# Performance work log

Hardware: AMD Instinct MI355X
Metric: run time of the kernel (lower is better)

The kernel has to match this reference:

```python
import jax, jax.numpy as jnp
import numpy as np

N = 200000   # 10000 graphs x 20 nodes, stacked
E = 3200000  # avg degree 16
F_IN = 4
H = 32
BN_EPS = 1e-5


def setup_inputs() -> dict:
    key = jax.random.key(0)
    ks = jax.random.split(key, 16)
    s = 0.1
    return {
        "x": jax.random.normal(ks[0], (N, F_IN), jnp.float32),
        "edge_index": jax.random.randint(ks[1], (2, E), 0, N, jnp.int64),
        "edge_weight": jax.random.uniform(ks[2], (E,), jnp.float32),
        "gcn1_w": jax.random.normal(ks[3], (F_IN, H), jnp.float32) * s,
        "gcn1_b": jnp.zeros((H,), jnp.float32),
        "gcn2_w": jax.random.normal(ks[4], (H, H), jnp.float32) * s,
        "gcn2_b": jnp.zeros((H,), jnp.float32),
        "bn1_gamma": jnp.ones((H,), jnp.float32),
        "bn1_beta": jnp.zeros((H,), jnp.float32),
        "bn1_mean": jnp.zeros((H,), jnp.float32),
        "bn1_var": jnp.ones((H,), jnp.float32),
        "bn2_gamma": jnp.ones((H,), jnp.float32),
        "bn2_beta": jnp.zeros((H,), jnp.float32),
        "bn2_mean": jnp.zeros((H,), jnp.float32),
        "bn2_var": jnp.ones((H,), jnp.float32),
        "lstm1_wih": jax.random.normal(ks[5], (4 * H, 2 * H), jnp.float32) * s,
        "lstm1_whh": jax.random.normal(ks[6], (4 * H, H), jnp.float32) * s,
        "lstm1_bih": jax.random.normal(ks[7], (4 * H,), jnp.float32) * s,
        "lstm1_bhh": jax.random.normal(ks[8], (4 * H,), jnp.float32) * s,
        "lstm2_wih": jax.random.normal(ks[9], (4 * H, H), jnp.float32) * s,
        "lstm2_whh": jax.random.normal(ks[10], (4 * H, H), jnp.float32) * s,
        "lstm2_bih": jax.random.normal(ks[11], (4 * H,), jnp.float32) * s,
        "lstm2_bhh": jax.random.normal(ks[12], (4 * H,), jnp.float32) * s,
        "lin_w": jax.random.normal(ks[13], (1, 2 * H + F_IN), jnp.float32) * s,
        "lin_b": jnp.zeros((1,), jnp.float32),
    }


def _gcn_conv(x, src, dst, ew, W, b, n):
    # GCNConv: x @ W, add self-loops (weight 1), symmetric normalization, scatter-add at dst.
    xw = x @ W
    loop = jnp.arange(n)
    s = jnp.concatenate([src, loop])
    d = jnp.concatenate([dst, loop])
    w = jnp.concatenate([ew, jnp.ones((n,), ew.dtype)])
    deg = jax.ops.segment_sum(w, d, num_segments=n)
    dinv = jnp.where(deg > 0, jax.lax.rsqrt(deg), 0.0)
    norm = dinv[s] * w * dinv[d]  # [E+N]
    out = jax.ops.segment_sum(norm[:, None] * xw[s], d, num_segments=n)
    return out + b


def _bn_eval(x, gamma, beta, mean, var):
    return (x - mean) * jax.lax.rsqrt(var + BN_EPS) * gamma + beta


def _lstm_step(x, wih, bih, bhh):
    # single timestep, zero initial (h, c): recurrent W_hh term vanishes.
    gates = x @ wih.T + bih + bhh
    i, f, g, o = jnp.split(gates, 4, axis=1)  # torch gate order i,f,g,o
    c = jax.nn.sigmoid(i) * jnp.tanh(g)
    return jax.nn.sigmoid(o) * jnp.tanh(c)


def reference(x, edge_index, edge_weight, gcn1_w, gcn1_b, gcn2_w, gcn2_b,
              bn1_gamma, bn1_beta, bn1_mean, bn1_var,
              bn2_gamma, bn2_beta, bn2_mean, bn2_var,
              lstm1_wih, lstm1_whh, lstm1_bih, lstm1_bhh,
              lstm2_wih, lstm2_whh, lstm2_bih, lstm2_bhh,
              lin_w, lin_b):
    n = x.shape[0]
    src, dst = edge_index[0], edge_index[1]
    # MPNNLSTM (window=1, eval mode: dropout=identity, BN uses running stats)
    h1 = _bn_eval(jax.nn.relu(_gcn_conv(x, src, dst, edge_weight, gcn1_w, gcn1_b, n)),
                  bn1_gamma, bn1_beta, bn1_mean, bn1_var)
    h2 = _bn_eval(jax.nn.relu(_gcn_conv(h1, src, dst, edge_weight, gcn2_w, gcn2_b, n)),
                  bn2_gamma, bn2_beta, bn2_mean, bn2_var)
    skip = jnp.concatenate([h1, h2], axis=1)  # [N, 2H]
    H1 = _lstm_step(skip, lstm1_wih, lstm1_bih, lstm1_bhh)  # [N, H]
    H2 = _lstm_step(H1, lstm2_wih, lstm2_bih, lstm2_bhh)    # [N, H]
    h = jnp.concatenate([H1, H2, x], axis=1)  # [N, 2H + F_IN]
    # RecurrentGCN head: relu + linear -> [N, 1]
    return jax.nn.relu(h) @ lin_w.T + lin_b
```

## Files before the change

kernel.cpp:

```cpp
#include <hip/hip_runtime.h>
#include <hip/hip_fp16.h>
#include <math.h>

#define BN_EPS 1e-5f
#define HF 32
#define BS 256
#define KEDGE 4096
#define MAXNB 800
#define WQ14 16383.0f
#define WQ22 4194303.0f

typedef _Float16 half8 __attribute__((ext_vector_type(8)));
typedef float f32x4 __attribute__((ext_vector_type(4)));
typedef float f32x2 __attribute__((ext_vector_type(2)));

__device__ __forceinline__ float fsig(float x) {
    return __builtin_amdgcn_rcpf(1.0f + __expf(-x));
}
__device__ __forceinline__ float ftanh(float x) {
    return 1.0f - 2.0f * __builtin_amdgcn_rcpf(1.0f + __expf(2.0f * x));
}


__device__ __forceinline__ float e4m3_to_f32_sw(unsigned v) {
    unsigned s = v & 0x80u, E = (v >> 3) & 0xFu, m = v & 7u;
    float r = E ? ldexpf((float)(8 + m), (int)E - 10) : ldexpf((float)m, -9);
    return s ? -r : r;
}

__device__ __forceinline__ unsigned f32_to_e4m3_sw(float x) {
    float ax = fabsf(x);
    unsigned s = x < 0.0f ? 0x80u : 0u;
    if (!(ax > 0.0f)) return s;
    if (ax >= 448.0f) return s | 0x7Eu;
    int e;
    float m = frexpf(ax, &e);
    int E = e - 1 + 7;
    if (E >= 1) {
        int q = (int)(m * 16.0f + 0.5f);
        if (q == 16) { q = 8; E += 1; if (E > 15) return s | 0x7Eu; }
        return s | (unsigned)(E << 3) | (unsigned)(q - 8);
    }
    int q = (int)(ax * 512.0f + 0.5f);
    if (q > 7) return s | 0x08u;
    return s | (unsigned)q;
}

__device__ __forceinline__ void dec8(uint2 r, float* f) {
#if __has_builtin(__builtin_amdgcn_cvt_pk_f32_fp8)
    f32x2 p0 = __builtin_amdgcn_cvt_pk_f32_fp8((int)r.x, false);
    f32x2 p1 = __builtin_amdgcn_cvt_pk_f32_fp8((int)r.x, true);
    f32x2 p2 = __builtin_amdgcn_cvt_pk_f32_fp8((int)r.y, false);
    f32x2 p3 = __builtin_amdgcn_cvt_pk_f32_fp8((int)r.y, true);
    f[0] = p0[0]; f[1] = p0[1]; f[2] = p1[0]; f[3] = p1[1];
    f[4] = p2[0]; f[5] = p2[1]; f[6] = p3[0]; f[7] = p3[1];
#else
#pragma unroll
    for (int k = 0; k < 4; ++k) f[k] = e4m3_to_f32_sw((r.x >> (8 * k)) & 0xFFu);
#pragma unroll
    for (int k = 0; k < 4; ++k) f[4 + k] = e4m3_to_f32_sw((r.y >> (8 * k)) & 0xFFu);
#endif
}

__device__ __forceinline__ uint2 enc8(const float* o) {
#if __has_builtin(__builtin_amdgcn_cvt_pk_fp8_f32)
    int w0 = 0, w1 = 0;
    w0 = __builtin_amdgcn_cvt_pk_fp8_f32(o[0], o[1], w0, false);
    w0 = __builtin_amdgcn_cvt_pk_fp8_f32(o[2], o[3], w0, true);
    w1 = __builtin_amdgcn_cvt_pk_fp8_f32(o[4], o[5], w1, false);
    w1 = __builtin_amdgcn_cvt_pk_fp8_f32(o[6], o[7], w1, true);
    return make_uint2((unsigned)w0, (unsigned)w1);
#else
    unsigned a = 0, b = 0;
#pragma unroll
    for (int k = 0; k < 4; ++k) a |= f32_to_e4m3_sw(o[k]) << (8 * k);
#pragma unroll
    for (int k = 0; k < 4; ++k) b |= f32_to_e4m3_sw(o[4 + k]) << (8 * k);
    return make_uint2(a, b);
#endif
}


__global__ __launch_bounds__(512) void k_binsort(
        const int* __restrict__ src, const int* __restrict__ dst,
        const float* __restrict__ ew, int E, int NB, int bcap,
        int* __restrict__ gcur, uint2* __restrict__ recs) {
    __shared__ uint2 srec[KEDGE];
    __shared__ int hist[MAXNB], excl[MAXNB], curs[MAXNB], sbase[MAXNB];

    int tid = threadIdx.x;
    int base = blockIdx.x * KEDGE;
    int cnt = min(KEDGE, E - base);

    for (int i = tid; i < NB; i += 512) hist[i] = 0;
    __syncthreads();

    for (int i = tid; i < cnt; i += 512)
        atomicAdd(&hist[dst[base + i] >> 8], 1);
    __syncthreads();

    if (tid < 64) {
        int run = 0;
        for (int c = 0; c < NB; c += 64) {
            int idx = c + tid;
            int v = (idx < NB) ? hist[idx] : 0;
            int incl = v;
#pragma unroll
            for (int o = 1; o < 64; o <<= 1) {
                int up = __shfl_up(incl, o, 64);
                if (tid >= o) incl += up;
            }
            if (idx < NB) { int e = run + incl - v; excl[idx] = e; curs[idx] = e; }
            run += __shfl(incl, 63, 64);
        }
    }
    __syncthreads();

    for (int i = tid; i < cnt; i += 512) {
        int s = src[base + i];
        int d = dst[base + i];
        float w = ew[base + i];
        unsigned q = (unsigned)(w * WQ22 + 0.5f);
        if (q > 4194303u) q = 4194303u;
        int b = d >> 8;
        int pos = atomicAdd(&curs[b], 1);
        srec[pos] = make_uint2(((unsigned)s << 8) | (unsigned)(d & 255),
                               ((unsigned)b << 22) | q);
    }
    __syncthreads();

    for (int b = tid; b < NB; b += 512) {
        int len = hist[b];
        sbase[b] = len ? atomicAdd(&gcur[b], len) : 0;
    }
    __syncthreads();

    for (int i = tid; i < cnt; i += 512) {
        uint2 u = srec[i];
        int b = u.y >> 22;
        int off = sbase[b] + (i - excl[b]);
        if (off < bcap) recs[(size_t)b * bcap + off] = u;
    }
}


__global__ __launch_bounds__(512) void k_sortb(
        const uint2* __restrict__ recs, const int* __restrict__ gcur,
        int bcap, int bcap4,
        const float* __restrict__ x, const float* __restrict__ W1,
        unsigned* __restrict__ recs4, int* __restrict__ pstart,
        int* __restrict__ pcnt, float* __restrict__ dinv,
        unsigned char* __restrict__ y18, int n) {
    __shared__ int hist[BS], excl4[BS], curs[BS], wsm[BS];
    __shared__ float sdv[BS];
    __shared__ float sW1[128];

    int b = blockIdx.x, tid = threadIdx.x;
    int cnt = min(gcur[b], bcap);
    const uint2* r = recs + (size_t)b * bcap;
    const float dq = 1.0f / WQ22;

    if (tid < BS) { hist[tid] = 0; wsm[tid] = 0; }
    if (tid >= 256 && tid < 384) sW1[tid - 256] = W1[tid - 256];
    __syncthreads();

    for (int i = tid; i < cnt; i += 512) {
        uint2 u = r[i];
        int dl = u.x & 255;
        atomicAdd(&hist[dl], 1);
        atomicAdd(&wsm[dl], (int)(u.y & 4194303u));
    }
    __syncthreads();

    if (tid < BS) {
        int g = b * BS + tid;
        sdv[tid] = (g < n) ? rsqrtf(1.0f + (float)wsm[tid] * dq) : 0.0f;
    }
    if (tid < 64) {
        int run = 0;
        for (int c = 0; c < BS; c += 64) {
            int idx = c + tid;
            int v = (hist[idx] + 3) & ~3;
            int incl = v;
#pragma unroll
            for (int o = 1; o < 64; o <<= 1) {
                int up = __shfl_up(incl, o, 64);
                if (tid >= o) incl += up;
            }
            int e = run + incl - v;
            excl4[idx] = e; curs[idx] = e;
            run += __shfl(incl, 63, 64);
        }
    }
    __syncthreads();

    unsigned* out4 = recs4 + (size_t)b * bcap4;
    for (int i = tid; i < cnt; i += 512) {
        uint2 u = r[i];
        int dl = u.x & 255;
        int pos = atomicAdd(&curs[dl], 1);
        float qn = (float)(u.y & 4194303u) * dq * sdv[dl];
        unsigned q = (unsigned)(qn * WQ14 + 0.5f);
        if (q > 16383u) q = 16383u;
        out4[pos] = ((u.x >> 8) << 14) | q;
    }

    {
        int node = tid >> 1, half = tid & 1;
        int g = b * BS + node;
        if (g < n) {
            float4 xv = *(const float4*)(x + (size_t)g * 4);
            float sc = sdv[node];
            int f0 = half * 16;
            float o[16];
#pragma unroll
            for (int k = 0; k < 16; ++k)
                o[k] = sc * (xv.x * sW1[f0 + k] + xv.y * sW1[32 + f0 + k] +
                             xv.z * sW1[64 + f0 + k] + xv.w * sW1[96 + f0 + k]);
            uint2 lo = enc8(o), hi = enc8(o + 8);
            *(uint4*)(y18 + ((size_t)g << 5) + half * 16) = make_uint4(lo.x, lo.y, hi.x, hi.y);
        }
    }

    if (tid < BS) {
        int g = b * BS + tid;
        if (g < n) {
            pstart[g] = b * bcap4 + excl4[tid];
            pcnt[g] = hist[tid];
            dinv[g] = sdv[tid];
        }
    }
}


__global__ __launch_bounds__(256) void k_prep(
        const float* __restrict__ wih1, const float* __restrict__ bih1,
        const float* __restrict__ bhh1, const float* __restrict__ wih2,
        const float* __restrict__ bih2, const float* __restrict__ bhh2,
        __half* __restrict__ wp1, __half* __restrict__ wp2,
        float* __restrict__ bsum1, float* __restrict__ bsum2,
        int* __restrict__ gcur, int NB) {
    const int tg[6] = {0, 16, 64, 80, 96, 112};
    int idx = blockIdx.x * 256 + threadIdx.x;
    if (idx < 6144) {
        int t = idx >> 10, rem = idx & 1023;
        int kc = rem >> 9, rem2 = rem & 511;
        int lane = rem2 >> 3, j = rem2 & 7;
        int g = tg[t] + (lane & 15);
        int k = kc * 32 + (lane >> 4) * 8 + j;
        wp1[idx] = __float2half(wih1[g * 64 + k]);
    } else if (idx < 9216) {
        int i2 = idx - 6144;
        int t = i2 >> 9, rem2 = i2 & 511;
        int lane = rem2 >> 3, j = rem2 & 7;
        int g = tg[t] + (lane & 15);
        int k = (lane >> 4) * 8 + j;
        wp2[i2] = __float2half(wih2[g * 32 + k]);
    } else if (idx < 9344) {
        int i = idx - 9216;
        bsum1[i] = bih1[i] + bhh1[i];
    } else if (idx < 9472) {
        int i = idx - 9344;
        bsum2[i] = bih2[i] + bhh2[i];
    } else if (idx < 9472 + NB) {
        gcur[idx - 9472] = 0;
    }
}


__global__ __launch_bounds__(256) void k_g1w2(
        const unsigned* __restrict__ recs4, const int* __restrict__ pstart,
        const int* __restrict__ pcnt, const float* __restrict__ dinv,
        const unsigned char* __restrict__ y18, const float* __restrict__ W2,
        const float* __restrict__ bias, const float* __restrict__ gamma,
        const float* __restrict__ beta, const float* __restrict__ mean,
        const float* __restrict__ var,
        __half* __restrict__ skiph, unsigned char* __restrict__ A8, int n) {
    __shared__ float sW2[1024];
    __shared__ float sh1[64][33];
    int tid = threadIdx.x;
    for (int i = tid; i < 1024; i += 256) sW2[i] = W2[i];
    __syncthreads();

    int nl = tid >> 2;
    int g = blockIdx.x * 64 + nl;
    int lane = tid & 3;
    int fq = lane * 8;
    bool act = g < n;

    float acc[8];
#pragma unroll
    for (int k = 0; k < 8; ++k) acc[k] = 0.0f;

    float dig = 0.0f;
    if (act) {
        dig = dinv[g];
        {
            uint2 sr = ((const uint2*)(y18 + ((size_t)g << 5)))[lane];
            float f[8];
            dec8(sr, f);
#pragma unroll
            for (int k = 0; k < 8; ++k) acc[k] = dig * f[k];
        }

        const float qs = 1.0f / WQ14;
        int cn = pcnt[g];
        const unsigned* r = recs4 + pstart[g];
        int e = 0;
        for (; e + 8 <= cn; e += 8) {
            uint4 ua = *(const uint4*)(r + e);
            uint4 ub = *(const uint4*)(r + e + 4);
            unsigned u[8] = {ua.x, ua.y, ua.z, ua.w, ub.x, ub.y, ub.z, ub.w};
            uint2 rw[8];
#pragma unroll
            for (int q = 0; q < 8; ++q)
                rw[q] = ((const uint2*)(y18 + ((size_t)(u[q] >> 14) << 5)))[lane];
            float nm[8];
#pragma unroll
            for (int q = 0; q < 8; ++q)
                nm[q] = (float)(u[q] & 16383u) * qs;
#pragma unroll
            for (int q = 0; q < 8; ++q) {
                float f[8];
                dec8(rw[q], f);
#pragma unroll
                for (int k = 0; k < 8; ++k) acc[k] += nm[q] * f[k];
            }
        }
        for (; e < cn; ++e) {
            unsigned u0 = r[e];
            uint2 r0 = ((const uint2*)(y18 + ((size_t)(u0 >> 14) << 5)))[lane];
            float n0 = (float)(u0 & 16383u) * qs;
            float f[8];
            dec8(r0, f);
#pragma unroll
            for (int k = 0; k < 8; ++k) acc[k] += n0 * f[k];
        }
    }

    float o[8];
#pragma unroll
    for (int k = 0; k < 8; ++k) {
        float v = fmaxf(acc[k] + bias[fq + k], 0.0f);
        o[k] = (v - mean[fq + k]) * gamma[fq + k] * rsqrtf(var[fq + k] + BN_EPS) + beta[fq + k];
        sh1[nl][fq + k] = o[k];
    }
    if (act) {
        union { __half h[8]; uint4 q; } hv;
#pragma unroll
        for (int k = 0; k < 8; ++k) hv.h[k] = __float2half(o[k]);
        *(uint4*)(skiph + (size_t)g * 64 + fq) = hv.q;
    }
    __syncthreads();

    if (act) {
        float a2[8];
#pragma unroll
        for (int j = 0; j < 8; ++j) a2[j] = 0.0f;
#pragma unroll 4
        for (int k = 0; k < 32; ++k) {
            float h = sh1[nl][k];
            const float* wr = sW2 + k * 32 + fq;
#pragma unroll
            for (int j = 0; j < 8; ++j) a2[j] += h * wr[j];
        }
#pragma unroll
        for (int j = 0; j < 8; ++j) a2[j] *= dig;
        ((uint2*)(A8 + ((size_t)g << 5)))[lane] = enc8(a2);
    }
}


__global__ __launch_bounds__(256) void k_gather8(
        const unsigned* __restrict__ recs4, const int* __restrict__ pstart,
        const int* __restrict__ pcnt, const float* __restrict__ dinv,
        const unsigned char* __restrict__ A8,
        const float* __restrict__ bias, const float* __restrict__ gamma,
        const float* __restrict__ beta, const float* __restrict__ mean,
        const float* __restrict__ var,
        __half* __restrict__ skiph, int uoff, int n) {
    int g = blockIdx.x * 64 + (threadIdx.x >> 2);
    int lane = threadIdx.x & 3;
    if (g >= n) return;

    float dig = dinv[g];
    float acc[8];
    {
        uint2 sr = ((const uint2*)(A8 + ((size_t)g << 5)))[lane];
        float f[8];
        dec8(sr, f);
#pragma unroll
        for (int k = 0; k < 8; ++k) acc[k] = dig * f[k];
    }

    const float qs = 1.0f / WQ14;
    int cn = pcnt[g];
    const unsigned* r = recs4 + pstart[g];
    int e = 0;
    for (; e + 8 <= cn; e += 8) {
        uint4 ua = *(const uint4*)(r + e);
        uint4 ub = *(const uint4*)(r + e + 4);
        unsigned u[8] = {ua.x, ua.y, ua.z, ua.w, ub.x, ub.y, ub.z, ub.w};
        uint2 rw[8];
#pragma unroll
        for (int q = 0; q < 8; ++q)
            rw[q] = ((const uint2*)(A8 + ((size_t)(u[q] >> 14) << 5)))[lane];
        float nm[8];
#pragma unroll
        for (int q = 0; q < 8; ++q)
            nm[q] = (float)(u[q] & 16383u) * qs;
#pragma unroll
        for (int q = 0; q < 8; ++q) {
            float f[8];
            dec8(rw[q], f);
#pragma unroll
            for (int k = 0; k < 8; ++k) acc[k] += nm[q] * f[k];
        }
    }
    for (; e < cn; ++e) {
        unsigned u0 = r[e];
        uint2 r0 = ((const uint2*)(A8 + ((size_t)(u0 >> 14) << 5)))[lane];
        float n0 = (float)(u0 & 16383u) * qs;
        float f0[8];
        dec8(r0, f0);
#pragma unroll
        for (int k = 0; k < 8; ++k) acc[k] += n0 * f0[k];
    }

    int fq = lane * 8;
    union { __half h[8]; uint4 q; } hv;
#pragma unroll
    for (int k = 0; k < 8; ++k) {
        float v = fmaxf(acc[k] + bias[fq + k], 0.0f);
        hv.h[k] = __float2half((v - mean[fq + k]) * gamma[fq + k] * rsqrtf(var[fq + k] + BN_EPS) + beta[fq + k]);
    }
    *(uint4*)(skiph + (size_t)g * 64 + uoff + fq) = hv.q;
}


__global__ __launch_bounds__(256) void k_headm(
        const __half* __restrict__ skiph, const float* __restrict__ x,
        const __half* __restrict__ wp1, const __half* __restrict__ wp2,
        const float* __restrict__ bsum1, const float* __restrict__ bsum2,
        const float* __restrict__ lw, const float* __restrict__ lb,
        float* __restrict__ out, int n) {
    __shared__ __align__(16) __half H1lds[4 * 16 * 40];
    int tid = threadIdx.x;
    int w = tid >> 6, l = tid & 63;
    int quad = l >> 4, c = l & 15;
    int node_base = blockIdx.x * 64 + w * 16;

    int arow = node_base + c; if (arow > n - 1) arow = n - 1;
    const half8* ap = (const half8*)(skiph + (size_t)arow * 64);
    half8 a0 = ap[quad];
    half8 a1 = ap[4 + quad];

    const half8* b1 = (const half8*)wp1;
    f32x4 d[6];
#pragma unroll
    for (int t = 0; t < 6; ++t) {
        f32x4 acc = {0.0f, 0.0f, 0.0f, 0.0f};
        acc = __builtin_amdgcn_mfma_f32_16x16x32_f16(a0, b1[(t * 2 + 0) * 64 + l], acc, 0, 0, 0);
        acc = __builtin_amdgcn_mfma_f32_16x16x32_f16(a1, b1[(t * 2 + 1) * 64 + l], acc, 0, 0, 0);
        d[t] = acc;
    }

    float bi0 = bsum1[c],      bi1 = bsum1[16 + c];
    float bg0 = bsum1[64 + c], bg1 = bsum1[80 + c];
    float bo0 = bsum1[96 + c], bo1 = bsum1[112 + c];
    float lwc0 = lw[c], lwc1 = lw[c + 16];

    float pa[4];
#pragma unroll
    for (int r = 0; r < 4; ++r) {
        float cc0 = fsig(d[0][r] + bi0) * ftanh(d[2][r] + bg0);
        float h0 = fsig(d[4][r] + bo0) * ftanh(cc0);
        float cc1 = fsig(d[1][r] + bi1) * ftanh(d[3][r] + bg1);
        float h1 = fsig(d[5][r] + bo1) * ftanh(cc1);
        pa[r] = fmaxf(h0, 0.0f) * lwc0 + fmaxf(h1, 0.0f) * lwc1;
        __half* hp = H1lds + (w * 16 + quad * 4 + r) * 40;
        hp[c] = __float2half(h0);
        hp[c + 16] = __float2half(h1);
    }
    __syncthreads();

    half8 a2 = *(const half8*)(H1lds + (w * 16 + c) * 40 + quad * 8);

    const half8* b2 = (const half8*)wp2;
    f32x4 e[6];
#pragma unroll
    for (int t = 0; t < 6; ++t) {
        f32x4 acc = {0.0f, 0.0f, 0.0f, 0.0f};
        e[t] = __builtin_amdgcn_mfma_f32_16x16x32_f16(a2, b2[t * 64 + l], acc, 0, 0, 0);
    }

    float ci0 = bsum2[c],      ci1 = bsum2[16 + c];
    float cg0 = bsum2[64 + c], cg1 = bsum2[80 + c];
    float co0 = bsum2[96 + c], co1 = bsum2[112 + c];
    float lw2c0 = lw[32 + c], lw2c1 = lw[48 + c];
#pragma unroll
    for (int r = 0; r < 4; ++r) {
        float cc0 = fsig(e[0][r] + ci0) * ftanh(e[2][r] + cg0);
        float h0 = fsig(e[4][r] + co0) * ftanh(cc0);
        float cc1 = fsig(e[1][r] + ci1) * ftanh(e[3][r] + cg1);
        float h1 = fsig(e[5][r] + co1) * ftanh(cc1);
        pa[r] += fmaxf(h0, 0.0f) * lw2c0 + fmaxf(h1, 0.0f) * lw2c1;
    }

#pragma unroll
    for (int m = 1; m < 16; m <<= 1) {
#pragma unroll
        for (int r = 0; r < 4; ++r) pa[r] += __shfl_xor(pa[r], m, 64);
    }

    if (c < 4) {
        int node = node_base + quad * 4 + c;
        if (node < n) {
            const float4 xv = *(const float4*)(x + (size_t)node * 4);
            out[node] = pa[c] + lb[0]
                + fmaxf(xv.x, 0.0f) * lw[64] + fmaxf(xv.y, 0.0f) * lw[65]
                + fmaxf(xv.z, 0.0f) * lw[66] + fmaxf(xv.w, 0.0f) * lw[67];
        }
    }
}


__global__ void k_initdeg(float* __restrict__ deg, int n) {
    int i = blockIdx.x * blockDim.x + threadIdx.x;
    if (i < n) deg[i] = 1.0f;
}

__global__ void k_deg_only(const int* __restrict__ dst, const float* __restrict__ ew,
                           float* __restrict__ deg, int E) {
    int e = blockIdx.x * blockDim.x + threadIdx.x;
    if (e < E) atomicAdd(&deg[dst[e]], ew[e]);
}

__global__ void k_dinv_f(float* __restrict__ deg, int n) {
    int i = blockIdx.x * blockDim.x + threadIdx.x;
    if (i < n) {
        float d = deg[i];
        deg[i] = d > 0.0f ? rsqrtf(d) : 0.0f;
    }
}

__global__ void k_xw1_f(const float* __restrict__ x, const float* __restrict__ W,
                        float* __restrict__ out, int n) {
    int idx = blockIdx.x * blockDim.x + threadIdx.x;
    if (idx >= n * HF) return;
    int nn = idx >> 5, f = idx & 31;
    const float4 xr = *(const float4*)(x + (size_t)nn * 4);
    out[idx] = xr.x * W[f] + xr.y * W[32 + f] + xr.z * W[64 + f] + xr.w * W[96 + f];
}

__global__ void k_xw2_f(const float* __restrict__ Hin, const float* __restrict__ W,
                        float* __restrict__ out, int n) {
    __shared__ float sW[32 * 32];
    __shared__ float sH[8][32];
    int tid = threadIdx.x;
    for (int i = tid; i < 1024; i += 256) sW[i] = W[i];
    int r = tid >> 5, f = tid & 31;
    int nn = blockIdx.x * 8 + r;
    if (nn < n) sH[r][f] = Hin[(size_t)nn * HF + f];
    __syncthreads();
    if (nn >= n) return;
    float acc = 0.0f;
#pragma unroll
    for (int k = 0; k < 32; ++k) acc += sH[r][k] * sW[k * 32 + f];
    out[(size_t)nn * HF + f] = acc;
}

__global__ void k_selfloop(const float* __restrict__ A, const float* __restrict__ dinv,
                           float* __restrict__ B, int n) {
    int idx = blockIdx.x * blockDim.x + threadIdx.x;
    if (idx >= n * HF) return;
    int nn = idx >> 5;
    float di = dinv[nn];
    B[idx] = di * di * A[idx];
}

__global__ void k_scatter(const int* __restrict__ src, const int* __restrict__ dst,
                          const float* __restrict__ ew, const float* __restrict__ dinv,
                          const float* __restrict__ A, float* __restrict__ B, int total) {
    int idx = blockIdx.x * blockDim.x + threadIdx.x;
    if (idx >= total) return;
    int e = idx >> 5, f = idx & 31;
    int s = src[e], d = dst[e];
    float norm = dinv[s] * ew[e] * dinv[d];
    atomicAdd(&B[d * HF + f], norm * A[s * HF + f]);
}

__global__ void k_post(const float* __restrict__ B, const float* __restrict__ bias,
                       const float* __restrict__ gamma, const float* __restrict__ beta,
                       const float* __restrict__ mean, const float* __restrict__ var,
                       float* __restrict__ Hout, int n) {
    int idx = blockIdx.x * blockDim.x + threadIdx.x;
    if (idx >= n * HF) return;
    int f = idx & 31;
    float v = fmaxf(B[idx] + bias[f], 0.0f);
    float sc = gamma[f] * rsqrtf(var[f] + BN_EPS);
    Hout[idx] = (v - mean[f]) * sc + beta[f];
}

__global__ __launch_bounds__(256) void k_head(
        const float* __restrict__ h1, const float* __restrict__ h2,
        const float* __restrict__ x,
        const float* __restrict__ wih1, const float* __restrict__ bih1, const float* __restrict__ bhh1,
        const float* __restrict__ wih2, const float* __restrict__ bih2, const float* __restrict__ bhh2,
        const float* __restrict__ lw, const float* __restrict__ lb,
        float* __restrict__ out, int n) {
    __shared__ float sH1[32 * 256];
    int tid = threadIdx.x;
    int nn = blockIdx.x * 256 + tid;
    if (nn >= n) return;

    const float4* a = (const float4*)(h1 + (size_t)nn * HF);
    const float4* b = (const float4*)(h2 + (size_t)nn * HF);
    float skip[64];
#pragma unroll
    for (int q = 0; q < 8; ++q) {
        float4 v = a[q];
        skip[4 * q] = v.x; skip[4 * q + 1] = v.y; skip[4 * q + 2] = v.z; skip[4 * q + 3] = v.w;
        float4 u = b[q];
        skip[32 + 4 * q] = u.x; skip[33 + 4 * q] = u.y; skip[34 + 4 * q] = u.z; skip[35 + 4 * q] = u.w;
    }

    float oa = lb[0];
#pragma unroll 1
    for (int j = 0; j < 32; ++j) {
        const float4* wi = (const float4*)(wih1 + (size_t)j * 64);
        const float4* wg = (const float4*)(wih1 + (size_t)(64 + j) * 64);
        const float4* wo = (const float4*)(wih1 + (size_t)(96 + j) * 64);
        float gi = bih1[j] + bhh1[j];
        float gg = bih1[64 + j] + bhh1[64 + j];
        float go = bih1[96 + j] + bhh1[96 + j];
#pragma unroll
        for (int q = 0; q < 16; ++q) {
            float4 aa = wi[q], bb = wg[q], cc4 = wo[q];
            float s0 = skip[4 * q], s1 = skip[4 * q + 1], s2 = skip[4 * q + 2], s3 = skip[4 * q + 3];
            gi += aa.x * s0 + aa.y * s1 + aa.z * s2 + aa.w * s3;
            gg += bb.x * s0 + bb.y * s1 + bb.z * s2 + bb.w * s3;
            go += cc4.x * s0 + cc4.y * s1 + cc4.z * s2 + cc4.w * s3;
        }
        float cc = fsig(gi) * ftanh(gg);
        float hh = fsig(go) * ftanh(cc);
        sH1[j * 256 + tid] = hh;
        oa += fmaxf(hh, 0.0f) * lw[j];
    }

#pragma unroll 1
    for (int j = 0; j < 32; ++j) {
        const float4* wi = (const float4*)(wih2 + (size_t)j * 32);
        const float4* wg = (const float4*)(wih2 + (size_t)(64 + j) * 32);
        const float4* wo = (const float4*)(wih2 + (size_t)(96 + j) * 32);
        float gi = bih2[j] + bhh2[j];
        float gg = bih2[64 + j] + bhh2[64 + j];
        float go = bih2[96 + j] + bhh2[96 + j];
#pragma unroll
        for (int q = 0; q < 8; ++q) {
            float4 aa = wi[q], bb = wg[q], cc4 = wo[q];
            float s0 = sH1[(4 * q) * 256 + tid], s1 = sH1[(4 * q + 1) * 256 + tid];
            float s2 = sH1[(4 * q + 2) * 256 + tid], s3 = sH1[(4 * q + 3) * 256 + tid];
            gi += aa.x * s0 + aa.y * s1 + aa.z * s2 + aa.w * s3;
            gg += bb.x * s0 + bb.y * s1 + bb.z * s2 + bb.w * s3;
            go += cc4.x * s0 + cc4.y * s1 + cc4.z * s2 + cc4.w * s3;
        }
        float cc = fsig(gi) * ftanh(gg);
        float hh = fsig(go) * ftanh(cc);
        oa += fmaxf(hh, 0.0f) * lw[32 + j];
    }

    const float4 xv = *(const float4*)(x + (size_t)nn * 4);
    oa += fmaxf(xv.x, 0.0f) * lw[64] + fmaxf(xv.y, 0.0f) * lw[65] +
          fmaxf(xv.z, 0.0f) * lw[66] + fmaxf(xv.w, 0.0f) * lw[67];
    out[nn] = oa;
}


extern "C" void kernel_launch(void* const* d_in, const int* in_sizes, int n_in,
                              void* d_out, int out_size, void* d_ws, size_t ws_size,
                              hipStream_t stream) {
    const float* x   = (const float*)d_in[0];
    const int*   ei  = (const int*)d_in[1];
    const float* ew  = (const float*)d_in[2];
    const float* g1w = (const float*)d_in[3];
    const float* g1b = (const float*)d_in[4];
    const float* g2w = (const float*)d_in[5];
    const float* g2b = (const float*)d_in[6];
    const float* bn1g = (const float*)d_in[7];
    const float* bn1b = (const float*)d_in[8];
    const float* bn1m = (const float*)d_in[9];
    const float* bn1v = (const float*)d_in[10];
    const float* bn2g = (const float*)d_in[11];
    const float* bn2b = (const float*)d_in[12];
    const float* bn2m = (const float*)d_in[13];
    const float* bn2v = (const float*)d_in[14];
    const float* w1ih = (const float*)d_in[15];
    const float* b1ih = (const float*)d_in[17];
    const float* b1hh = (const float*)d_in[18];
    const float* w2ih = (const float*)d_in[19];
    const float* b2ih = (const float*)d_in[21];
    const float* b2hh = (const float*)d_in[22];
    const float* lw   = (const float*)d_in[23];
    const float* lb   = (const float*)d_in[24];
    float* out = (float*)d_out;

    const int N = in_sizes[0] / 4;
    const int E = in_sizes[2];
    const int* src = ei;
    const int* dst = ei + E;

    const int T = 256;
    const int NB = (N + BS - 1) / BS;
    long long meanb = ((long long)BS * E) / (N > 0 ? N : 1);
    int bcap = (int)(meanb + meanb / 4 + 128);
    bcap = (bcap + 3) & ~3;
    int bcap4 = bcap + 3 * BS;

    char* p = (char*)d_ws;
    auto alloc = [&](size_t bytes) { char* q = p; p += (bytes + 255) & ~(size_t)255; return q; };
    int*      gcur   = (int*)alloc(sizeof(int) * NB);
    uint2*    recs   = (uint2*)alloc(sizeof(uint2) * (size_t)NB * bcap);
    unsigned* recs4  = (unsigned*)alloc(sizeof(unsigned) * (size_t)NB * bcap4);
    float*    dinv   = (float*)alloc(sizeof(float) * N);
    int*      pstart = (int*)alloc(sizeof(int) * N);
    int*      pcnt   = (int*)alloc(sizeof(int) * N);
    unsigned char* y18 = (unsigned char*)alloc((size_t)N * HF);
    unsigned char* A8  = (unsigned char*)alloc((size_t)N * HF);
    __half*   skiph  = (__half*)alloc(sizeof(__half) * (size_t)N * 64);
    __half*   wp1    = (__half*)alloc(sizeof(__half) * 6144);
    __half*   wp2    = (__half*)alloc(sizeof(__half) * 3072);
    float*    bsum1  = (float*)alloc(sizeof(float) * 128);
    float*    bsum2  = (float*)alloc(sizeof(float) * 128);
    size_t need = (size_t)(p - (char*)d_ws);

    int bN  = (N + T - 1) / T;
    int bE  = (E + T - 1) / T;
    int bNF = (N * HF + T - 1) / T;
    int bN8 = (N + 7) / 8;
    int bG  = (N + 63) / 64;
    int bBin = (E + KEDGE - 1) / KEDGE;
    int bPrep = (9472 + NB + 255) / 256;

    if (ws_size >= need && NB <= MAXNB && N <= (1 << 18)) {
        k_prep<<<bPrep, 256, 0, stream>>>(w1ih, b1ih, b1hh, w2ih, b2ih, b2hh,
                                          wp1, wp2, bsum1, bsum2, gcur, NB);
        k_binsort<<<bBin, 512, 0, stream>>>(src, dst, ew, E, NB, bcap, gcur, recs);
        k_sortb<<<NB, 512, 0, stream>>>(recs, gcur, bcap, bcap4, x, g1w,
                                        recs4, pstart, pcnt, dinv, y18, N);

        k_g1w2<<<bG, T, 0, stream>>>(recs4, pstart, pcnt, dinv, y18, g2w,
                                     g1b, bn1g, bn1b, bn1m, bn1v, skiph, A8, N);
        k_gather8<<<bG, T, 0, stream>>>(recs4, pstart, pcnt, dinv, A8,
                                        g2b, bn2g, bn2b, bn2m, bn2v, skiph, 32, N);
        k_headm<<<bG, T, 0, stream>>>(skiph, x, wp1, wp2, bsum1, bsum2,
                                      lw, lb, out, N);
    } else {
        size_t Npad = ((size_t)N + 255) & ~(size_t)255;
        float* fdinv = (float*)d_ws;
        float* fA = fdinv + Npad;
        float* fB = fA + (size_t)N * HF;
        float* fC = fB + (size_t)N * HF;
        int bEF = (int)(((long long)E * HF + T - 1) / T);
        int bH = (N + 255) / 256;

        k_initdeg<<<bN, T, 0, stream>>>(fdinv, N);
        k_deg_only<<<bE, T, 0, stream>>>(dst, ew, fdinv, E);
        k_dinv_f<<<bN, T, 0, stream>>>(fdinv, N);

        k_xw1_f<<<bNF, T, 0, stream>>>(x, g1w, fA, N);
        k_selfloop<<<bNF, T, 0, stream>>>(fA, fdinv, fB, N);
        k_scatter<<<bEF, T, 0, stream>>>(src, dst, ew, fdinv, fA, fB, E * HF);
        k_post<<<bNF, T, 0, stream>>>(fB, g1b, bn1g, bn1b, bn1m, bn1v, fC, N);

        k_xw2_f<<<bN8, T, 0, stream>>>(fC, g2w, fA, N);
        k_selfloop<<<bNF, T, 0, stream>>>(fA, fdinv, fB, N);
        k_scatter<<<bEF, T, 0, stream>>>(src, dst, ew, fdinv, fA, fB, E * HF);
        k_post<<<bNF, T, 0, stream>>>(fB, g2b, bn2g, bn2b, bn2m, bn2v, fB, N);

        k_head<<<bH, T, 0, stream>>>(fC, fB, x, w1ih, b1ih, b1hh, w2ih, b2ih, b2hh,
                                     lw, lb, out, N);
    }
}
```

Baseline: 299.1 us.

## Bin edges via register-held records instead of LDS staging sort

The edge binning kernel now keeps each thread's 8 packed edge records in registers and reads src/dst/weight only once, building the histogram in the same pass. It drops the LDS record buffer, the wave-level prefix scan and the second global read. Scatter offsets now come from per-bin atomics on a shared cursor seeded from the global reservation. This frees about 32KB of shared memory, which should raise occupancy and cut a pass. In exchange, records within a bin are no longer grouped contiguously in shared memory, so global writes may coalesce less well and shared atomic contention rises.

```diff
diff --git a/kernel.cpp b/kernel.cpp
--- a/kernel.cpp
+++ b/kernel.cpp
@@ -85,8 +85,7 @@
         const int* __restrict__ src, const int* __restrict__ dst,
         const float* __restrict__ ew, int E, int NB, int bcap,
         int* __restrict__ gcur, uint2* __restrict__ recs) {
-    __shared__ uint2 srec[KEDGE];
-    __shared__ int hist[MAXNB], excl[MAXNB], curs[MAXNB], sbase[MAXNB];
+    __shared__ int hist[MAXNB], curs[MAXNB];
 
     int tid = threadIdx.x;
     int base = blockIdx.x * KEDGE;
@@ -95,51 +94,39 @@
     for (int i = tid; i < NB; i += 512) hist[i] = 0;
     __syncthreads();
 
-    for (int i = tid; i < cnt; i += 512)
-        atomicAdd(&hist[dst[base + i] >> 8], 1);
-    __syncthreads();
-
-    if (tid < 64) {
-        int run = 0;
-        for (int c = 0; c < NB; c += 64) {
-            int idx = c + tid;
-            int v = (idx < NB) ? hist[idx] : 0;
-            int incl = v;
-#pragma unroll
-            for (int o = 1; o < 64; o <<= 1) {
-                int up = __shfl_up(incl, o, 64);
-                if (tid >= o) incl += up;
-            }
-            if (idx < NB) { int e = run + incl - v; excl[idx] = e; curs[idx] = e; }
-            run += __shfl(incl, 63, 64);
-        }
-    }
-    __syncthreads();
-
-    for (int i = tid; i < cnt; i += 512) {
-        int s = src[base + i];
-        int d = dst[base + i];
-        float w = ew[base + i];
-        unsigned q = (unsigned)(w * WQ22 + 0.5f);
-        if (q > 4194303u) q = 4194303u;
-        int b = d >> 8;
-        int pos = atomicAdd(&curs[b], 1);
-        srec[pos] = make_uint2(((unsigned)s << 8) | (unsigned)(d & 255),
-                               ((unsigned)b << 22) | q);
+    uint2 rec[KEDGE / 512];
+#pragma unroll
+    for (int k = 0; k < KEDGE / 512; ++k) {
+        int i = tid + k * 512;
+        if (i < cnt) {
+            int s = src[base + i];
+            int d = dst[base + i];
+            float w = ew[base + i];
+            unsigned q = (unsigned)(w * WQ22 + 0.5f);
+            if (q > 4194303u) q = 4194303u;
+            int b = d >> 8;
+            rec[k] = make_uint2(((unsigned)s << 8) | (unsigned)(d & 255),
+                                ((unsigned)b << 22) | q);
+            atomicAdd(&hist[b], 1);
+        }
     }
     __syncthreads();
 
     for (int b = tid; b < NB; b += 512) {
         int len = hist[b];
-        sbase[b] = len ? atomicAdd(&gcur[b], len) : 0;
-    }
-    __syncthreads();
-
-    for (int i = tid; i < cnt; i += 512) {
-        uint2 u = srec[i];
-        int b = u.y >> 22;
-        int off = sbase[b] + (i - excl[b]);
-        if (off < bcap) recs[(size_t)b * bcap + off] = u;
+        curs[b] = len ? atomicAdd(&gcur[b], len) : 0;
+    }
+    __syncthreads();
+
+#pragma unroll
+    for (int k = 0; k < KEDGE / 512; ++k) {
+        int i = tid + k * 512;
+        if (i < cnt) {
+            uint2 u = rec[k];
+            int b = u.y >> 22;
+            int off = atomicAdd(&curs[b], 1);
+            if (off < bcap) recs[(size_t)b * bcap + off] = u;
+        }
     }
 }
 
```

Result: no change. 296.9 us (-0.8%).
